# Kernel tuning notes

Hardware: AMD Instinct MI355X
Metric: run time of the kernel (lower is better)

Reference implementation:

```python
import jax, jax.numpy as jnp
import numpy as np

B = 65536
SD1, SD2 = 256, 256
IN_D, OUT_D = 128, 128
NL_IN, NL_HID, NL_OUT = 256, 1024, 256


def setup_inputs() -> dict:
    key = jax.random.key(0)
    ks = jax.random.split(key, 16)
    s = lambda k, shape: jax.random.normal(k, shape, dtype=jnp.float32) * (1.0 / np.sqrt(shape[-1]))
    return {
        "state1": jax.random.normal(ks[0], (B, SD1), dtype=jnp.float32),
        "state2": jax.random.normal(ks[1], (B, SD2), dtype=jnp.float32),
        "u": jax.random.normal(ks[2], (B, IN_D), dtype=jnp.float32),
        # First linear block (Wiener)
        "A1": s(ks[3], (SD1, SD1)),
        "B1": s(ks[4], (SD1, IN_D)),
        "C1": s(ks[5], (NL_IN, SD1)),
        "D1": s(ks[6], (NL_IN, IN_D)),
        # Second linear block (Hammerstein)
        "A2": s(ks[7], (SD2, SD2)),
        "B2": s(ks[8], (SD2, NL_OUT)),
        "C2": s(ks[9], (OUT_D, SD2)),
        "D2": s(ks[10], (OUT_D, NL_OUT)),
        # CustomNonlinearity: 2-layer tanh MLP 256 -> 1024 -> 256
        "W1": s(ks[11], (NL_HID, NL_IN)),
        "b1": jnp.zeros((NL_HID,), dtype=jnp.float32),
        "W2": s(ks[12], (NL_OUT, NL_HID)),
        "b2": jnp.zeros((NL_OUT,), dtype=jnp.float32),
    }


def nonlinearity(v, W1, b1, W2, b2):
    return jnp.tanh(v @ W1.T + b1) @ W2.T + b2


def reference(state1, state2, u, A1, B1, C1, D1, A2, B2, C2, D2, W1, b1, W2, b2):
    next_state1 = state1 @ A1.T + u @ B1.T            # [B, SD1]
    v = state1 @ C1.T + u @ D1.T                      # [B, NL_IN]
    w = nonlinearity(v, W1, b1, W2, b2)               # [B, NL_OUT]
    next_state2 = state2 @ A2.T + w @ B2.T            # [B, SD2]
    y = state2 @ C2.T + w @ D2.T                      # [B, OUT_D]
    return (next_state1, next_state2, y)
```

## Files before the change

kernel.cpp:

```cpp
#include <hip/hip_runtime.h>

#define NB 65536

typedef __attribute__((ext_vector_type(8))) short bf16x8;
typedef __attribute__((ext_vector_type(4))) float f32x4;

__device__ __forceinline__ unsigned short f2bf(float f) {
  union { float f; unsigned u; } v; v.f = f;
  return (unsigned short)((v.u + 0x7FFFu + ((v.u >> 16) & 1u)) >> 16);
}

#define OFF_A1 0
#define OFF_B1 65536
#define OFF_C1 98304
#define OFF_D1 163840
#define OFF_A2 196608
#define OFF_B2 262144
#define OFF_C2 327680
#define OFF_D2 360448
#define OFF_W1 393216
#define OFF_W2 655360
#define W_TOTAL 917504

struct WPtrs { const float* p[10]; };

__global__ void convert_weights(WPtrs wp, unsigned short* __restrict__ dst) {
  const int off[11] = {OFF_A1, OFF_B1, OFF_C1, OFF_D1, OFF_A2, OFF_B2,
                       OFF_C2, OFF_D2, OFF_W1, OFF_W2, W_TOTAL};
  int gid4 = (blockIdx.x * blockDim.x + threadIdx.x) * 4;
  if (gid4 >= W_TOTAL) return;
  int seg = 0;
  #pragma unroll
  for (int i = 1; i < 10; ++i) seg += (gid4 >= off[i]) ? 1 : 0;
  const float4 f = *(const float4*)(wp.p[seg] + (gid4 - off[seg]));
  ushort4 h;
  h.x = f2bf(f.x); h.y = f2bf(f.y); h.z = f2bf(f.z); h.w = f2bf(f.w);
  *(ushort4*)(dst + gid4) = h;
}

#define MFMA16(acc, a, b) \
  acc = __builtin_amdgcn_mfma_f32_16x16x32_bf16(a, b, acc, 0, 0, 0)

#define CLD 72
#define VLD 264
#define HLD 136
#define SMEM_BYTES (18432 + 67584 + 34816)

__global__ __launch_bounds__(512, 2) void wh_fused(
    const float* __restrict__ s1, const float* __restrict__ s2,
    const float* __restrict__ u, const unsigned short* __restrict__ wbf,
    const float* __restrict__ b1, const float* __restrict__ b2,
    float* __restrict__ out)
{
  extern __shared__ char smem[];
  unsigned short* chunk = (unsigned short*)smem;
  unsigned short* vbuf  = (unsigned short*)(smem + 18432);
  unsigned short* hbuf  = (unsigned short*)(smem + 18432 + 67584);

  const int t   = threadIdx.x;
  const int wid = t >> 6;
  const int lid = t & 63;
  const int lr  = lid & 15;
  const int lg  = lid >> 4;
  const int row0 = blockIdx.x * 128;

  auto stage = [&](const float* __restrict__ src, int sld, int c0) {
    const int cg = t & 15;
    const int r0 = t >> 4;
    #pragma unroll
    for (int rr = 0; rr < 128; rr += 32) {
      const float4 f = *(const float4*)(src + (size_t)(row0 + r0 + rr) * sld + c0 + cg * 4);
      ushort4 h;
      h.x = f2bf(f.x); h.y = f2bf(f.y); h.z = f2bf(f.z); h.w = f2bf(f.w);
      *(ushort4*)(chunk + (r0 + rr) * CLD + cg * 4) = h;
    }
  };

  auto ldsA = [&](const unsigned short* buf, int ld, int m, int kk) -> bf16x8 {
    return *(const bf16x8*)(buf + (m * 16 + lr) * ld + kk + lg * 8);
  };
  auto ldgB = [&](const unsigned short* w, int ld, int nrow, int kk) -> bf16x8 {
    return *(const bf16x8*)(w + (size_t)(nrow + lr) * ld + kk + lg * 8);
  };

  f32x4 ns1[8][2] = {};
  f32x4 vac[8][2] = {};
  for (int c = 0; c < 6; ++c) {
    __syncthreads();
    if (c < 4) stage(s1, 256, c * 64); else stage(u, 128, (c - 4) * 64);
    __syncthreads();
    const unsigned short* WA = wbf + (c < 4 ? OFF_A1 : OFF_B1);
    const unsigned short* WC = wbf + (c < 4 ? OFF_C1 : OFF_D1);
    const int wld   = (c < 4) ? 256 : 128;
    const int kbase = (c < 4) ? c * 64 : (c - 4) * 64;
    #pragma unroll
    for (int k2 = 0; k2 < 2; ++k2) {
      bf16x8 a[8];
      #pragma unroll
      for (int m = 0; m < 8; ++m) a[m] = ldsA(chunk, CLD, m, k2 * 32);
      #pragma unroll
      for (int n = 0; n < 2; ++n) {
        bf16x8 ba = ldgB(WA, wld, wid * 32 + n * 16, kbase + k2 * 32);
        bf16x8 bc = ldgB(WC, wld, wid * 32 + n * 16, kbase + k2 * 32);
        #pragma unroll
        for (int m = 0; m < 8; ++m) {
          MFMA16(ns1[m][n], a[m], ba);
          MFMA16(vac[m][n], a[m], bc);
        }
      }
    }
  }
  #pragma unroll
  for (int m = 0; m < 8; ++m)
    #pragma unroll
    for (int n = 0; n < 2; ++n)
      #pragma unroll
      for (int i = 0; i < 4; ++i)
        out[(size_t)(row0 + m * 16 + lg * 4 + i) * 256 + wid * 32 + n * 16 + lr] = ns1[m][n][i];
  #pragma unroll
  for (int m = 0; m < 8; ++m)
    #pragma unroll
    for (int n = 0; n < 2; ++n)
      #pragma unroll
      for (int i = 0; i < 4; ++i)
        vbuf[(m * 16 + lg * 4 + i) * VLD + wid * 32 + n * 16 + lr] = f2bf(vac[m][n][i]);
  __syncthreads();

  f32x4 wac[8][2] = {};
  for (int hc = 0; hc < 8; ++hc) {
    f32x4 hac[8] = {};
    for (int k = 0; k < 8; ++k) {
      bf16x8 a[8];
      #pragma unroll
      for (int m = 0; m < 8; ++m) a[m] = ldsA(vbuf, VLD, m, k * 32);
      bf16x8 bw = ldgB(wbf + OFF_W1, 256, hc * 128 + wid * 16, k * 32);
      #pragma unroll
      for (int m = 0; m < 8; ++m) MFMA16(hac[m], a[m], bw);
    }
    const float bias1 = b1[hc * 128 + wid * 16 + lr];
    __syncthreads();
    #pragma unroll
    for (int m = 0; m < 8; ++m)
      #pragma unroll
      for (int i = 0; i < 4; ++i)
        hbuf[(m * 16 + lg * 4 + i) * HLD + wid * 16 + lr] = f2bf(tanhf(hac[m][i] + bias1));
    __syncthreads();
    for (int k = 0; k < 4; ++k) {
      bf16x8 a[8];
      #pragma unroll
      for (int m = 0; m < 8; ++m) a[m] = ldsA(hbuf, HLD, m, k * 32);
      #pragma unroll
      for (int n = 0; n < 2; ++n) {
        bf16x8 b2f = ldgB(wbf + OFF_W2, 1024, wid * 32 + n * 16, hc * 128 + k * 32);
        #pragma unroll
        for (int m = 0; m < 8; ++m) MFMA16(wac[m][n], a[m], b2f);
      }
    }
  }
  #pragma unroll
  for (int m = 0; m < 8; ++m)
    #pragma unroll
    for (int n = 0; n < 2; ++n) {
      const float bias2 = b2[wid * 32 + n * 16 + lr];
      #pragma unroll
      for (int i = 0; i < 4; ++i)
        vbuf[(m * 16 + lg * 4 + i) * VLD + wid * 32 + n * 16 + lr] = f2bf(wac[m][n][i] + bias2);
    }
  __syncthreads();

  f32x4 ns2[8][2] = {};
  f32x4 yac[8] = {};
  for (int c = 0; c < 4; ++c) {
    __syncthreads();
    stage(s2, 256, c * 64);
    __syncthreads();
    #pragma unroll
    for (int k2 = 0; k2 < 2; ++k2) {
      bf16x8 a[8];
      #pragma unroll
      for (int m = 0; m < 8; ++m) a[m] = ldsA(chunk, CLD, m, k2 * 32);
      const int kk = c * 64 + k2 * 32;
      bf16x8 by = ldgB(wbf + OFF_C2, 256, wid * 16, kk);
      #pragma unroll
      for (int n = 0; n < 2; ++n) {
        bf16x8 ba = ldgB(wbf + OFF_A2, 256, wid * 32 + n * 16, kk);
        #pragma unroll
        for (int m = 0; m < 8; ++m) MFMA16(ns2[m][n], a[m], ba);
      }
      #pragma unroll
      for (int m = 0; m < 8; ++m) MFMA16(yac[m], a[m], by);
    }
  }
  for (int k = 0; k < 8; ++k) {
    bf16x8 a[8];
    #pragma unroll
    for (int m = 0; m < 8; ++m) a[m] = ldsA(vbuf, VLD, m, k * 32);
    bf16x8 by = ldgB(wbf + OFF_D2, 256, wid * 16, k * 32);
    #pragma unroll
    for (int n = 0; n < 2; ++n) {
      bf16x8 bb = ldgB(wbf + OFF_B2, 256, wid * 32 + n * 16, k * 32);
      #pragma unroll
      for (int m = 0; m < 8; ++m) MFMA16(ns2[m][n], a[m], bb);
    }
    #pragma unroll
    for (int m = 0; m < 8; ++m) MFMA16(yac[m], a[m], by);
  }
  float* out2 = out + (size_t)NB * 256;
  float* outy = out + (size_t)NB * 512;
  #pragma unroll
  for (int m = 0; m < 8; ++m)
    #pragma unroll
    for (int n = 0; n < 2; ++n)
      #pragma unroll
      for (int i = 0; i < 4; ++i)
        out2[(size_t)(row0 + m * 16 + lg * 4 + i) * 256 + wid * 32 + n * 16 + lr] = ns2[m][n][i];
  #pragma unroll
  for (int m = 0; m < 8; ++m)
    #pragma unroll
    for (int i = 0; i < 4; ++i)
      outy[(size_t)(row0 + m * 16 + lg * 4 + i) * 128 + wid * 16 + lr] = yac[m][i];
}

extern "C" void kernel_launch(void* const* d_in, const int* in_sizes, int n_in,
                              void* d_out, int out_size, void* d_ws, size_t ws_size,
                              hipStream_t stream) {
  const float* s1 = (const float*)d_in[0];
  const float* s2 = (const float*)d_in[1];
  const float* u  = (const float*)d_in[2];
  WPtrs wp;
  wp.p[0] = (const float*)d_in[3];
  wp.p[1] = (const float*)d_in[4];
  wp.p[2] = (const float*)d_in[5];
  wp.p[3] = (const float*)d_in[6];
  wp.p[4] = (const float*)d_in[7];
  wp.p[5] = (const float*)d_in[8];
  wp.p[6] = (const float*)d_in[9];
  wp.p[7] = (const float*)d_in[10];
  wp.p[8] = (const float*)d_in[11];
  wp.p[9] = (const float*)d_in[13];
  const float* b1 = (const float*)d_in[12];
  const float* b2 = (const float*)d_in[14];
  unsigned short* wbf = (unsigned short*)d_ws;

  convert_weights<<<dim3((W_TOTAL / 4 + 511) / 512), dim3(512), 0, stream>>>(wp, wbf);
  wh_fused<<<dim3(NB / 128), dim3(512), SMEM_BYTES, stream>>>(
      s1, s2, u, wbf, b1, b2, (float*)d_out);
}
```

Before: 249.4 us.

## Warp-specialize MLP stages, double-buffer staging, fast tanh and packed bf16 conversion

New measurement: 411.9 us. 65.2% more time.

```diff
diff --git a/kernel.cpp b/kernel.cpp
--- a/kernel.cpp
+++ b/kernel.cpp
@@ -5,9 +5,19 @@
 typedef __attribute__((ext_vector_type(8))) short bf16x8;
 typedef __attribute__((ext_vector_type(4))) float f32x4;
 
+__device__ __forceinline__ unsigned cvtpk(float lo, float hi) {
+  unsigned r;
+  asm("v_cvt_pk_bf16_f32 %0, %1, %2" : "=v"(r) : "v"(lo), "v"(hi));
+  return r;
+}
 __device__ __forceinline__ unsigned short f2bf(float f) {
   union { float f; unsigned u; } v; v.f = f;
   return (unsigned short)((v.u + 0x7FFFu + ((v.u >> 16) & 1u)) >> 16);
+}
+__device__ __forceinline__ float fast_tanh(float x) {
+  float e = __builtin_amdgcn_exp2f(__builtin_fabsf(x) * -2.885390081777927f);
+  float t = (1.0f - e) * __builtin_amdgcn_rcpf(1.0f + e);
+  return __builtin_copysignf(t, x);
 }
 
 #define OFF_A1 0
@@ -33,9 +43,10 @@
   #pragma unroll
   for (int i = 1; i < 10; ++i) seg += (gid4 >= off[i]) ? 1 : 0;
   const float4 f = *(const float4*)(wp.p[seg] + (gid4 - off[seg]));
-  ushort4 h;
-  h.x = f2bf(f.x); h.y = f2bf(f.y); h.z = f2bf(f.z); h.w = f2bf(f.w);
-  *(ushort4*)(dst + gid4) = h;
+  uint2 h;
+  h.x = cvtpk(f.x, f.y);
+  h.y = cvtpk(f.z, f.w);
+  *(uint2*)(dst + gid4) = h;
 }
 
 #define MFMA16(acc, a, b) \
@@ -44,7 +55,7 @@
 #define CLD 72
 #define VLD 264
 #define HLD 136
-#define SMEM_BYTES (18432 + 67584 + 34816)
+#define SMEM_BYTES (67584 + 2*34816)
 
 __global__ __launch_bounds__(512, 2) void wh_fused(
     const float* __restrict__ s1, const float* __restrict__ s2,
@@ -53,29 +64,38 @@
     float* __restrict__ out)
 {
   extern __shared__ char smem[];
-  unsigned short* chunk = (unsigned short*)smem;
-  unsigned short* vbuf  = (unsigned short*)(smem + 18432);
-  unsigned short* hbuf  = (unsigned short*)(smem + 18432 + 67584);
+  unsigned short* vbuf = (unsigned short*)smem;
+  unsigned short* hbp[2];
+  hbp[0] = (unsigned short*)(smem + 67584);
+  hbp[1] = (unsigned short*)(smem + 67584 + 34816);
+  unsigned short* cbp[2];
+  cbp[0] = (unsigned short*)(smem + 67584);
+  cbp[1] = (unsigned short*)(smem + 67584 + 18432);
 
   const int t   = threadIdx.x;
-  const int wid = t >> 6;
+  const int wc  = t >> 6;
   const int lid = t & 63;
   const int lr  = lid & 15;
   const int lg  = lid >> 4;
   const int row0 = blockIdx.x * 128;
 
-  auto stage = [&](const float* __restrict__ src, int sld, int c0) {
-    const int cg = t & 15;
-    const int r0 = t >> 4;
+  float4 st[4];
+  auto stageLoad = [&](const float* __restrict__ src, int sld, int c0) {
+    const int cg = t & 15, r0 = t >> 4;
     #pragma unroll
-    for (int rr = 0; rr < 128; rr += 32) {
-      const float4 f = *(const float4*)(src + (size_t)(row0 + r0 + rr) * sld + c0 + cg * 4);
-      ushort4 h;
-      h.x = f2bf(f.x); h.y = f2bf(f.y); h.z = f2bf(f.z); h.w = f2bf(f.w);
-      *(ushort4*)(chunk + (r0 + rr) * CLD + cg * 4) = h;
-    }
+    for (int rr = 0; rr < 4; ++rr)
+      st[rr] = *(const float4*)(src + (size_t)(row0 + r0 + rr * 32) * sld + c0 + cg * 4);
   };
-
+  auto stageWrite = [&](unsigned short* dst) {
+    const int cg = t & 15, r0 = t >> 4;
+    #pragma unroll
+    for (int rr = 0; rr < 4; ++rr) {
+      uint2 h;
+      h.x = cvtpk(st[rr].x, st[rr].y);
+      h.y = cvtpk(st[rr].z, st[rr].w);
+      *(uint2*)(dst + (r0 + rr * 32) * CLD + cg * 4) = h;
+    }
+  };
   auto ldsA = [&](const unsigned short* buf, int ld, int m, int kk) -> bf16x8 {
     return *(const bf16x8*)(buf + (m * 16 + lr) * ld + kk + lg * 8);
   };
@@ -83,142 +103,179 @@
     return *(const bf16x8*)(w + (size_t)(nrow + lr) * ld + kk + lg * 8);
   };
 
-  f32x4 ns1[8][2] = {};
-  f32x4 vac[8][2] = {};
-  for (int c = 0; c < 6; ++c) {
+  f32x4 acc[8][4] = {};
+  {
+    const unsigned short* Wk1 = wbf + (wc < 4 ? OFF_A1 : OFF_C1);
+    const unsigned short* Wk2 = wbf + (wc < 4 ? OFF_B1 : OFF_D1);
+    const int cb4 = (wc & 3) * 64;
+    stageLoad(s1, 256, 0);
+    stageWrite(cbp[0]);
     __syncthreads();
-    if (c < 4) stage(s1, 256, c * 64); else stage(u, 128, (c - 4) * 64);
+    for (int c = 0; c < 6; ++c) {
+      if (c < 5) {
+        if (c + 1 < 4) stageLoad(s1, 256, (c + 1) * 64);
+        else           stageLoad(u, 128, (c + 1 - 4) * 64);
+      }
+      const unsigned short* W = (c < 4) ? Wk1 : Wk2;
+      const int wld = (c < 4) ? 256 : 128;
+      const int kb  = (c < 4) ? c * 64 : (c - 4) * 64;
+      const unsigned short* cbuf = cbp[c & 1];
+      #pragma unroll
+      for (int k2 = 0; k2 < 2; ++k2) {
+        bf16x8 a[8];
+        #pragma unroll
+        for (int m = 0; m < 8; ++m) a[m] = ldsA(cbuf, CLD, m, k2 * 32);
+        #pragma unroll
+        for (int n = 0; n < 4; ++n) {
+          bf16x8 b = ldgB(W, wld, cb4 + n * 16, kb + k2 * 32);
+          #pragma unroll
+          for (int m = 0; m < 8; ++m) MFMA16(acc[m][n], a[m], b);
+        }
+      }
+      if (c < 5) stageWrite(cbp[(c + 1) & 1]);
+      __syncthreads();
+    }
+    if (wc < 4) {
+      #pragma unroll
+      for (int m = 0; m < 8; ++m)
+        #pragma unroll
+        for (int n = 0; n < 4; ++n)
+          #pragma unroll
+          for (int i = 0; i < 4; ++i)
+            out[(size_t)(row0 + m * 16 + lg * 4 + i) * 256 + wc * 64 + n * 16 + lr] = acc[m][n][i];
+    } else {
+      #pragma unroll
+      for (int m = 0; m < 8; ++m)
+        #pragma unroll
+        for (int n = 0; n < 4; ++n)
+          #pragma unroll
+          for (int i = 0; i < 4; ++i)
+            vbuf[(m * 16 + lg * 4 + i) * VLD + (wc - 4) * 64 + n * 16 + lr] = f2bf(acc[m][n][i]);
+    }
     __syncthreads();
-    const unsigned short* WA = wbf + (c < 4 ? OFF_A1 : OFF_B1);
-    const unsigned short* WC = wbf + (c < 4 ? OFF_C1 : OFF_D1);
-    const int wld   = (c < 4) ? 256 : 128;
-    const int kbase = (c < 4) ? c * 64 : (c - 4) * 64;
+  }
+
+  f32x4 wac[8][4] = {};
+  {
+    const int pq = wc & 3;
+    for (int s = 0; s < 9; ++s) {
+      if (wc >= 4 && s < 8) {
+        f32x4 hac[8][2] = {};
+        #pragma unroll
+        for (int k = 0; k < 8; ++k) {
+          bf16x8 a[8];
+          #pragma unroll
+          for (int m = 0; m < 8; ++m) a[m] = ldsA(vbuf, VLD, m, k * 32);
+          #pragma unroll
+          for (int n = 0; n < 2; ++n) {
+            bf16x8 b = ldgB(wbf + OFF_W1, 256, s * 128 + pq * 32 + n * 16, k * 32);
+            #pragma unroll
+            for (int m = 0; m < 8; ++m) MFMA16(hac[m][n], a[m], b);
+          }
+        }
+        unsigned short* hb = hbp[s & 1];
+        #pragma unroll
+        for (int n = 0; n < 2; ++n) {
+          const float b1v = b1[s * 128 + pq * 32 + n * 16 + lr];
+          #pragma unroll
+          for (int m = 0; m < 8; ++m)
+            #pragma unroll
+            for (int i = 0; i < 4; ++i)
+              hb[(m * 16 + lg * 4 + i) * HLD + pq * 32 + n * 16 + lr] =
+                  f2bf(fast_tanh(hac[m][n][i] + b1v));
+        }
+      }
+      if (wc < 4 && s >= 1) {
+        const unsigned short* hb = hbp[(s - 1) & 1];
+        #pragma unroll
+        for (int k = 0; k < 4; ++k) {
+          bf16x8 a[8];
+          #pragma unroll
+          for (int m = 0; m < 8; ++m) a[m] = ldsA(hb, HLD, m, k * 32);
+          #pragma unroll
+          for (int n = 0; n < 4; ++n) {
+            bf16x8 b = ldgB(wbf + OFF_W2, 1024, wc * 64 + n * 16, (s - 1) * 128 + k * 32);
+            #pragma unroll
+            for (int m = 0; m < 8; ++m) MFMA16(wac[m][n], a[m], b);
+          }
+        }
+      }
+      __syncthreads();
+    }
+    if (wc < 4) {
+      #pragma unroll
+      for (int n = 0; n < 4; ++n) {
+        const float b2v = b2[wc * 64 + n * 16 + lr];
+        #pragma unroll
+        for (int m = 0; m < 8; ++m)
+          #pragma unroll
+          for (int i = 0; i < 4; ++i)
+            vbuf[(m * 16 + lg * 4 + i) * VLD + wc * 64 + n * 16 + lr] =
+                f2bf(wac[m][n][i] + b2v);
+      }
+    }
+    __syncthreads();
+  }
+
+  f32x4 cac[8][3] = {};
+  {
+    stageLoad(s2, 256, 0);
+    stageWrite(cbp[0]);
+    __syncthreads();
+    for (int c = 0; c < 4; ++c) {
+      if (c < 3) stageLoad(s2, 256, (c + 1) * 64);
+      const unsigned short* cbuf = cbp[c & 1];
+      #pragma unroll
+      for (int k2 = 0; k2 < 2; ++k2) {
+        bf16x8 a[8];
+        #pragma unroll
+        for (int m = 0; m < 8; ++m) a[m] = ldsA(cbuf, CLD, m, k2 * 32);
+        const int kk = c * 64 + k2 * 32;
+        #pragma unroll
+        for (int n = 0; n < 3; ++n) {
+          const int cg = wc * 48 + n * 16;
+          const unsigned short* W = (cg < 256)
+              ? (wbf + OFF_A2 + (size_t)cg * 256)
+              : (wbf + OFF_C2 + (size_t)(cg - 256) * 256);
+          bf16x8 b = *(const bf16x8*)(W + (size_t)lr * 256 + kk + lg * 8);
+          #pragma unroll
+          for (int m = 0; m < 8; ++m) MFMA16(cac[m][n], a[m], b);
+        }
+      }
+      if (c < 3) stageWrite(cbp[(c + 1) & 1]);
+      __syncthreads();
+    }
     #pragma unroll
-    for (int k2 = 0; k2 < 2; ++k2) {
-      bf16x8 a[8];
-      #pragma unroll
-      for (int m = 0; m < 8; ++m) a[m] = ldsA(chunk, CLD, m, k2 * 32);
-      #pragma unroll
-      for (int n = 0; n < 2; ++n) {
-        bf16x8 ba = ldgB(WA, wld, wid * 32 + n * 16, kbase + k2 * 32);
-        bf16x8 bc = ldgB(WC, wld, wid * 32 + n * 16, kbase + k2 * 32);
-        #pragma unroll
-        for (int m = 0; m < 8; ++m) {
-          MFMA16(ns1[m][n], a[m], ba);
-          MFMA16(vac[m][n], a[m], bc);
-        }
-      }
-    }
-  }
-  #pragma unroll
-  for (int m = 0; m < 8; ++m)
-    #pragma unroll
-    for (int n = 0; n < 2; ++n)
-      #pragma unroll
-      for (int i = 0; i < 4; ++i)
-        out[(size_t)(row0 + m * 16 + lg * 4 + i) * 256 + wid * 32 + n * 16 + lr] = ns1[m][n][i];
-  #pragma unroll
-  for (int m = 0; m < 8; ++m)
-    #pragma unroll
-    for (int n = 0; n < 2; ++n)
-      #pragma unroll
-      for (int i = 0; i < 4; ++i)
-        vbuf[(m * 16 + lg * 4 + i) * VLD + wid * 32 + n * 16 + lr] = f2bf(vac[m][n][i]);
-  __syncthreads();
-
-  f32x4 wac[8][2] = {};
-  for (int hc = 0; hc < 8; ++hc) {
-    f32x4 hac[8] = {};
     for (int k = 0; k < 8; ++k) {
       bf16x8 a[8];
       #pragma unroll
       for (int m = 0; m < 8; ++m) a[m] = ldsA(vbuf, VLD, m, k * 32);
-      bf16x8 bw = ldgB(wbf + OFF_W1, 256, hc * 128 + wid * 16, k * 32);
-      #pragma unroll
-      for (int m = 0; m < 8; ++m) MFMA16(hac[m], a[m], bw);
-    }
-    const float bias1 = b1[hc * 128 + wid * 16 + lr];
-    __syncthreads();
+      #pragma unroll
+      for (int n = 0; n < 3; ++n) {
+        const int cg = wc * 48 + n * 16;
+        const unsigned short* W = (cg < 256)
+            ? (wbf + OFF_B2 + (size_t)cg * 256)
+            : (wbf + OFF_D2 + (size_t)(cg - 256) * 256);
+        bf16x8 b = *(const bf16x8*)(W + (size_t)lr * 256 + k * 32 + lg * 8);
+        #pragma unroll
+        for (int m = 0; m < 8; ++m) MFMA16(cac[m][n], a[m], b);
+      }
+    }
+    float* out2 = out + (size_t)NB * 256;
+    float* outy = out + (size_t)NB * 512;
     #pragma unroll
-    for (int m = 0; m < 8; ++m)
-      #pragma unroll
-      for (int i = 0; i < 4; ++i)
-        hbuf[(m * 16 + lg * 4 + i) * HLD + wid * 16 + lr] = f2bf(tanhf(hac[m][i] + bias1));
-    __syncthreads();
-    for (int k = 0; k < 4; ++k) {
-      bf16x8 a[8];
-      #pragma unroll
-      for (int m = 0; m < 8; ++m) a[m] = ldsA(hbuf, HLD, m, k * 32);
-      #pragma unroll
-      for (int n = 0; n < 2; ++n) {
-        bf16x8 b2f = ldgB(wbf + OFF_W2, 1024, wid * 32 + n * 16, hc * 128 + k * 32);
-        #pragma unroll
-        for (int m = 0; m < 8; ++m) MFMA16(wac[m][n], a[m], b2f);
-      }
+    for (int n = 0; n < 3; ++n) {
+      const int cg = wc * 48 + n * 16;
+      #pragma unroll
+      for (int m = 0; m < 8; ++m)
+        #pragma unroll
+        for (int i = 0; i < 4; ++i) {
+          const size_t row = row0 + m * 16 + lg * 4 + i;
+          if (cg < 256) out2[row * 256 + cg + lr] = cac[m][n][i];
+          else          outy[row * 128 + cg - 256 + lr] = cac[m][n][i];
+        }
     }
   }
-  #pragma unroll
-  for (int m = 0; m < 8; ++m)
-    #pragma unroll
-    for (int n = 0; n < 2; ++n) {
-      const float bias2 = b2[wid * 32 + n * 16 + lr];
-      #pragma unroll
-      for (int i = 0; i < 4; ++i)
-        vbuf[(m * 16 + lg * 4 + i) * VLD + wid * 32 + n * 16 + lr] = f2bf(wac[m][n][i] + bias2);
-    }
-  __syncthreads();
-
-  f32x4 ns2[8][2] = {};
-  f32x4 yac[8] = {};
-  for (int c = 0; c < 4; ++c) {
-    __syncthreads();
-    stage(s2, 256, c * 64);
-    __syncthreads();
-    #pragma unroll
-    for (int k2 = 0; k2 < 2; ++k2) {
-      bf16x8 a[8];
-      #pragma unroll
-      for (int m = 0; m < 8; ++m) a[m] = ldsA(chunk, CLD, m, k2 * 32);
-      const int kk = c * 64 + k2 * 32;
-      bf16x8 by = ldgB(wbf + OFF_C2, 256, wid * 16, kk);
-      #pragma unroll
-      for (int n = 0; n < 2; ++n) {
-        bf16x8 ba = ldgB(wbf + OFF_A2, 256, wid * 32 + n * 16, kk);
-        #pragma unroll
-        for (int m = 0; m < 8; ++m) MFMA16(ns2[m][n], a[m], ba);
-      }
-      #pragma unroll
-      for (int m = 0; m < 8; ++m) MFMA16(yac[m], a[m], by);
-    }
-  }
-  for (int k = 0; k < 8; ++k) {
-    bf16x8 a[8];
-    #pragma unroll
-    for (int m = 0; m < 8; ++m) a[m] = ldsA(vbuf, VLD, m, k * 32);
-    bf16x8 by = ldgB(wbf + OFF_D2, 256, wid * 16, k * 32);
-    #pragma unroll
-    for (int n = 0; n < 2; ++n) {
-      bf16x8 bb = ldgB(wbf + OFF_B2, 256, wid * 32 + n * 16, k * 32);
-      #pragma unroll
-      for (int m = 0; m < 8; ++m) MFMA16(ns2[m][n], a[m], bb);
-    }
-    #pragma unroll
-    for (int m = 0; m < 8; ++m) MFMA16(yac[m], a[m], by);
-  }
-  float* out2 = out + (size_t)NB * 256;
-  float* outy = out + (size_t)NB * 512;
-  #pragma unroll
-  for (int m = 0; m < 8; ++m)
-    #pragma unroll
-    for (int n = 0; n < 2; ++n)
-      #pragma unroll
-      for (int i = 0; i < 4; ++i)
-        out2[(size_t)(row0 + m * 16 + lg * 4 + i) * 256 + wid * 32 + n * 16 + lr] = ns2[m][n][i];
-  #pragma unroll
-  for (int m = 0; m < 8; ++m)
-    #pragma unroll
-    for (int i = 0; i < 4; ++i)
-      outy[(size_t)(row0 + m * 16 + lg * 4 + i) * 128 + wid * 16 + lr] = yac[m][i];
 }
 
 extern "C" void kernel_launch(void* const* d_in, const int* in_sizes, int n_in,
```
